# Optimization experiments

Hardware: AMD Instinct MI355X
Metric: run time of the kernel (lower is better)

The kernel has to match this reference:

```python
import jax, jax.numpy as jnp
import numpy as np

EMB = 1024
HEADS = 16
HEAD_DIM = EMB // HEADS


def setup_inputs() -> dict:
    key = jax.random.key(0)
    ks = jax.random.split(key, 6)
    B, S = 4, 1024
    inputs = jax.random.normal(ks[0], (B, S, EMB), dtype=jnp.float32)
    # causal mask: 1.0 where attention is disallowed (added * -1e9 in the layer)
    mask = (1.0 - jnp.tril(jnp.ones((S, S), dtype=jnp.float32)))[None, None, :, :]
    scale = 1.0 / np.sqrt(EMB)
    wq = jax.random.normal(ks[1], (EMB, EMB), dtype=jnp.float32) * scale
    wk = jax.random.normal(ks[2], (EMB, EMB), dtype=jnp.float32) * scale
    wv = jax.random.normal(ks[3], (EMB, EMB), dtype=jnp.float32) * scale
    wo = jax.random.normal(ks[4], (EMB, EMB), dtype=jnp.float32) * scale
    zb = jnp.zeros((EMB,), dtype=jnp.float32)
    return {"inputs": inputs, "mask": mask, "wq": wq, "bq": zb, "wk": wk,
            "bk": zb, "wv": wv, "bv": zb, "wo": wo, "bo": zb}


def _split_heads(t, B):
    # [B, S, E] -> [B, H, S, Dh]
    return t.reshape(B, -1, HEADS, HEAD_DIM).transpose(0, 2, 1, 3)


def reference(inputs, mask, wq, bq, wk, bk, wv, bv, wo, bo):
    B = inputs.shape[0]
    q = _split_heads(inputs @ wq + bq, B)
    k = _split_heads(inputs @ wk + bk, B)
    v = _split_heads(inputs @ wv + bv, B)
    # NOTE: source divides by sqrt(sqrt(head_num)) = head_num**0.25
    scores = jnp.einsum('bhsd,bhtd->bhst', q, k) / jnp.asarray(HEADS, inputs.dtype) ** 0.25
    if mask is not None:
        scores = scores + mask * -1e9
    attn = jax.nn.softmax(scores, axis=-1)
    z = jnp.einsum('bhst,bhtd->bhsd', attn, v)
    # Faithful to source: reshape [B,H,S,Dh] -> [B,S,E] WITHOUT transposing heads back
    z = z.reshape(B, -1, EMB)
    return z @ wo + bo
```

## Files before the change

kernel.cpp:

```cpp
#include <hip/hip_runtime.h>
#include <hip/hip_bf16.h>
#include <stdint.h>

typedef __attribute__((ext_vector_type(8))) short short8;
typedef __attribute__((ext_vector_type(4))) float float4v;

#define SEQ   1024
#define NQKV  3072

__device__ __forceinline__ float bf2f(ushort h) {
    union { uint u; float f; } c; c.u = ((uint)h) << 16; return c.f;
}
__device__ __forceinline__ ushort f2bf(float f) {
    union { uint u; float f; } c; c.f = f;
    uint u = c.u;
    return (ushort)((u + 0x7fffu + ((u >> 16) & 1u)) >> 16);
}
__device__ __forceinline__ uint cvt_pk_bf16(float lo, float hi) {
    uint r;
    asm volatile("v_cvt_pk_bf16_f32 %0, %1, %2" : "=v"(r) : "v"(lo), "v"(hi));
    return r;
}
__device__ __forceinline__ void gl2lds16(const ushort* g, ushort* l) {
    __builtin_amdgcn_global_load_lds(
        (const __attribute__((address_space(1))) unsigned int*)(g),
        (__attribute__((address_space(3))) unsigned int*)(l),
        16, 0, 0);
}

#define FENCE() asm volatile("" ::: "memory")
#define PBAR()  do { FENCE(); __builtin_amdgcn_s_barrier(); FENCE(); } while (0)

__global__ __launch_bounds__(256) void prep_k(const void* __restrict__ X,
                                              const void* __restrict__ w0,
                                              const void* __restrict__ w1,
                                              const void* __restrict__ w2,
                                              const void* __restrict__ w3,
                                              const void* __restrict__ bq,
                                              const void* __restrict__ bk,
                                              const void* __restrict__ bv,
                                              const void* __restrict__ bo,
                                              ushort* __restrict__ xc,
                                              ushort* __restrict__ biasout,
                                              ushort* __restrict__ wtall,
                                              int* __restrict__ flag) {
    __shared__ int tot;
    __shared__ ushort tile[64][72];
    int t = threadIdx.x;
    if (t == 0) tot = 0;
    __syncthreads();
    uint wv = ((const uint*)X)[t];
    uint e = (wv >> 7) & 0xFFu;
    bool isbf = (e >= 100u && e <= 130u);
    unsigned long long m = __ballot(isbf);
    if ((t & 63) == 0) atomicAdd(&tot, __popcll(m));
    __syncthreads();
    bool isf = (tot <= 128);

    int bi = blockIdx.x;
    if (bi == 0 && t == 0) flag[0] = isf ? 1 : 0;

    if (bi < 4096) {
        if (!isf) return;
        int i = (bi * 256 + t) * 4;
        float4 v = *(const float4*)((const float*)X + i);
        ushort4 o;
        o.x = f2bf(v.x); o.y = f2bf(v.y); o.z = f2bf(v.z); o.w = f2bf(v.w);
        *(ushort4*)(xc + i) = o;
    } else if (bi < 4112) {
        int i = (bi - 4096) * 256 + t;
        int sel = i >> 10, j = i & 1023;
        const void* p = (sel == 0) ? bq : (sel == 1) ? bk : (sel == 2) ? bv : bo;
        biasout[i] = isf ? f2bf(((const float*)p)[j]) : ((const ushort*)p)[j];
    } else {
        int idx = bi - 4112;
        int z = idx >> 8, rem = idx & 255;
        const void* in = (z == 0) ? w0 : (z == 1) ? w1 : (z == 2) ? w2 : w3;
        ushort* out = wtall + (size_t)z * 1024 * 1024;
        int k0 = (rem & 15) * 64, n0 = (rem >> 4) * 64;
        int r = t >> 3, c = (t & 7) * 8;
#pragma unroll
        for (int p = 0; p < 2; p++) {
            int rr = r + p * 32;
            if (isf) {
                const float* src = (const float*)in + (size_t)(k0 + rr) * 1024 + n0 + c;
                float4 v0 = *(const float4*)src;
                float4 v1 = *(const float4*)(src + 4);
                tile[rr][c + 0] = f2bf(v0.x); tile[rr][c + 1] = f2bf(v0.y);
                tile[rr][c + 2] = f2bf(v0.z); tile[rr][c + 3] = f2bf(v0.w);
                tile[rr][c + 4] = f2bf(v1.x); tile[rr][c + 5] = f2bf(v1.y);
                tile[rr][c + 6] = f2bf(v1.z); tile[rr][c + 7] = f2bf(v1.w);
            } else {
                uint4 v = *(const uint4*)((const ushort*)in + (size_t)(k0 + rr) * 1024 + n0 + c);
                *(uint4*)&tile[rr][c] = v;
            }
        }
        __syncthreads();
#pragma unroll
        for (int p = 0; p < 2; p++) {
            int n = r + p * 32;
            ushort vals[8];
#pragma unroll
            for (int j = 0; j < 8; j++) vals[j] = tile[c + j][n];
            *(uint4*)(out + (size_t)(n0 + n) * 1024 + k0 + c) = *(uint4*)vals;
        }
    }
}

__device__ __forceinline__ void stage_half(const ushort* src, int K, ushort* lds, int t) {
#pragma unroll
    for (int jj = 0; jj < 2; jj++) {
        int c = jj * 512 + t;
        int row = c >> 3, s = c & 7;
        int kc = s ^ (row & 7);
        gl2lds16(src + (size_t)row * K + kc * 8, lds + c * 8);
    }
}

__global__ __launch_bounds__(512, 2) void gemm256_k(const ushort* __restrict__ Araw,
                                                    const ushort* __restrict__ Aconv,
                                                    const ushort* __restrict__ BT,
                                                    const ushort* __restrict__ bias,
                                                    ushort* __restrict__ C,
                                                    ushort* __restrict__ vt,
                                                    const int* __restrict__ flag) {
    constexpr int K = 1024;
    constexpr int N = NQKV;
    __shared__ ushort As[2][256 * 64];
    __shared__ ushort Bs[2][256 * 64];
    int orig = blockIdx.y * gridDim.x + blockIdx.x;
    int swz = (orig & 7) * 24 + (orig >> 3);
    int n0 = (swz % 12) * 256, m0 = (swz / 12) * 256;
    int t = threadIdx.x;
    int w = t >> 6, lane = t & 63, q = lane >> 4, ln = lane & 15;
    int wr = w & 1, wc = w >> 1;
    const ushort* A = (*flag) ? Aconv : Araw;

    float4v acc[8][4];
#pragma unroll
    for (int r = 0; r < 8; r++)
#pragma unroll
        for (int cc = 0; cc < 4; cc++) acc[r][cc] = (float4v){0.f, 0.f, 0.f, 0.f};

    stage_half(A  + (size_t)m0 * K,           K, &As[0][0], t);
    stage_half(A  + (size_t)(m0 + 128) * K,   K, &As[0][128 * 64], t);
    stage_half(BT + (size_t)n0 * K,           K, &Bs[0][0], t);
    stage_half(BT + (size_t)(n0 + 128) * K,   K, &Bs[0][128 * 64], t);
    stage_half(A  + (size_t)m0 * K + 64,      K, &As[1][0], t);
    stage_half(A  + (size_t)(m0 + 128) * K + 64, K, &As[1][128 * 64], t);
    asm volatile("s_waitcnt vmcnt(4)" ::: "memory");
    PBAR();

    short8 af[4][2];
    short8 bf[2][2][2];

    for (int j = 0; j < 16; j++) {
        int cur = j & 1;
        int nxt = cur ^ 1;
#pragma unroll
        for (int mf = 0; mf < 4; mf++)
#pragma unroll
            for (int kh = 0; kh < 2; kh++) {
                int r = wr * 64 + mf * 16 + ln;
                af[mf][kh] = *(const short8*)&As[cur][(r * 8 + ((kh * 4 + q) ^ (r & 7))) * 8];
            }
#pragma unroll
        for (int nf = 0; nf < 2; nf++)
#pragma unroll
            for (int kh = 0; kh < 2; kh++) {
                int rb = wc * 64 + nf * 16 + ln;
                bf[0][nf][kh] = *(const short8*)&Bs[cur][(rb * 8 + ((kh * 4 + q) ^ (rb & 7))) * 8];
            }
        if (j + 1 < 16) stage_half(BT + (size_t)n0 * K + (j + 1) * 64, K, &Bs[nxt][0], t);
#pragma unroll
        for (int mf = 0; mf < 4; mf++)
#pragma unroll
            for (int nf = 0; nf < 2; nf++)
#pragma unroll
                for (int kh = 0; kh < 2; kh++)
                    acc[mf][nf] = __builtin_amdgcn_mfma_f32_16x16x32_bf16(af[mf][kh], bf[0][nf][kh], acc[mf][nf], 0, 0, 0);
        PBAR();
#pragma unroll
        for (int nf = 0; nf < 2; nf++)
#pragma unroll
            for (int kh = 0; kh < 2; kh++) {
                int rb = wc * 64 + 32 + nf * 16 + ln;
                bf[1][nf][kh] = *(const short8*)&Bs[cur][(rb * 8 + ((kh * 4 + q) ^ (rb & 7))) * 8];
            }
        if (j + 1 < 16) stage_half(BT + (size_t)(n0 + 128) * K + (j + 1) * 64, K, &Bs[nxt][128 * 64], t);
#pragma unroll
        for (int mf = 0; mf < 4; mf++)
#pragma unroll
            for (int nf = 0; nf < 2; nf++)
#pragma unroll
                for (int kh = 0; kh < 2; kh++)
                    acc[mf][2 + nf] = __builtin_amdgcn_mfma_f32_16x16x32_bf16(af[mf][kh], bf[1][nf][kh], acc[mf][2 + nf], 0, 0, 0);
        PBAR();
#pragma unroll
        for (int mf = 0; mf < 4; mf++)
#pragma unroll
            for (int kh = 0; kh < 2; kh++) {
                int r = 128 + wr * 64 + mf * 16 + ln;
                af[mf][kh] = *(const short8*)&As[cur][(r * 8 + ((kh * 4 + q) ^ (r & 7))) * 8];
            }
        if (j + 2 < 16) stage_half(A + (size_t)m0 * K + (j + 2) * 64, K, &As[cur][0], t);
#pragma unroll
        for (int mf = 0; mf < 4; mf++)
#pragma unroll
            for (int nf = 0; nf < 2; nf++)
#pragma unroll
                for (int kh = 0; kh < 2; kh++)
                    acc[4 + mf][2 + nf] = __builtin_amdgcn_mfma_f32_16x16x32_bf16(af[mf][kh], bf[1][nf][kh], acc[4 + mf][2 + nf], 0, 0, 0);
        PBAR();
        if (j + 2 < 16) stage_half(A + (size_t)(m0 + 128) * K + (j + 2) * 64, K, &As[cur][128 * 64], t);
#pragma unroll
        for (int mf = 0; mf < 4; mf++)
#pragma unroll
            for (int nf = 0; nf < 2; nf++)
#pragma unroll
                for (int kh = 0; kh < 2; kh++)
                    acc[4 + mf][nf] = __builtin_amdgcn_mfma_f32_16x16x32_bf16(af[mf][kh], bf[0][nf][kh], acc[4 + mf][nf], 0, 0, 0);
        if (j < 14) { asm volatile("s_waitcnt vmcnt(4)" ::: "memory"); }
        else        { asm volatile("s_waitcnt vmcnt(0)" ::: "memory"); }
        PBAR();
    }

    bool wrv = (n0 >= 2048);
#pragma unroll
    for (int nfull = 0; nfull < 4; nfull++) {
        int n = n0 + wc * 64 + nfull * 16 + ln;
        float bs = bf2f(bias[n]);
#pragma unroll
        for (int m8 = 0; m8 < 8; m8++) {
            ushort pk[4];
#pragma unroll
            for (int i = 0; i < 4; i++) {
                int m = m0 + (m8 >> 2) * 128 + wr * 64 + (m8 & 3) * 16 + q * 4 + i;
                float v = acc[m8][nfull][i] + bs;
                C[(size_t)m * N + n] = f2bf(v);
                pk[i] = f2bf(v);
            }
            if (wrv) {
                int mb = m0 + (m8 >> 2) * 128 + wr * 64 + (m8 & 3) * 16 + q * 4;
                int b = mb >> 10, trow = mb & 1023;
                int h = (n - 2048) >> 6, d = n & 63;
                *(ushort4*)(vt + (((size_t)(b * 16 + h) * 64 + d) * 1024 + trow)) = *(ushort4*)pk;
            }
        }
    }
}

template <int BM, bool DUAL, bool WRV>
__global__ __launch_bounds__(256) void gemm_k(const ushort* __restrict__ Araw,
                                              const ushort* __restrict__ Aconv,
                                              const ushort* __restrict__ BT,
                                              const ushort* __restrict__ bias,
                                              void* __restrict__ C,
                                              ushort* __restrict__ vt,
                                              const int* __restrict__ flag,
                                              int M, int N, int K) {
    constexpr int RM = BM / 32;
    constexpr int AJ = BM / 64;
    __shared__ ushort As[2][BM * 32];
    __shared__ ushort Bs[2][128 * 32];
    int nwgx = gridDim.x;
    int orig = blockIdx.y * nwgx + blockIdx.x;
    int cpx = (nwgx * gridDim.y) >> 3;
    int swz = (orig & 7) * cpx + (orig >> 3);
    int n0 = (swz % nwgx) * 128, m0 = (swz / nwgx) * BM;
    int t = threadIdx.x;
    int w = t >> 6, lane = t & 63, q = lane >> 4, ln = lane & 15;
    int wr = w >> 1, wc = w & 1;
    const ushort* A = (*flag) ? Aconv : Araw;

    float4v acc[RM][4];
#pragma unroll
    for (int r = 0; r < RM; r++)
#pragma unroll
        for (int cc = 0; cc < 4; cc++) acc[r][cc] = (float4v){0.f, 0.f, 0.f, 0.f};

#pragma unroll
    for (int j = 0; j < AJ; j++) {
        int c = j * 256 + t;
        int row = c >> 2, s = c & 3;
        int kc = s ^ ((row >> 1) & 3);
        gl2lds16(A + (size_t)(m0 + row) * K + kc * 8, &As[0][c * 8]);
    }
#pragma unroll
    for (int j = 0; j < 2; j++) {
        int c = j * 256 + t;
        int row = c >> 2, s = c & 3;
        int kc = s ^ ((row >> 1) & 3);
        gl2lds16(BT + (size_t)(n0 + row) * K + kc * 8, &Bs[0][c * 8]);
    }

    int nIter = K >> 5;
    for (int kt = 0; kt < nIter; kt++) {
        int cur = kt & 1;
        __syncthreads();
        if (kt + 1 < nIter) {
            int nk0 = (kt + 1) << 5, nxt = cur ^ 1;
#pragma unroll
            for (int j = 0; j < AJ; j++) {
                int c = j * 256 + t;
                int row = c >> 2, s = c & 3;
                int kc = s ^ ((row >> 1) & 3);
                gl2lds16(A + (size_t)(m0 + row) * K + nk0 + kc * 8, &As[nxt][c * 8]);
            }
#pragma unroll
            for (int j = 0; j < 2; j++) {
                int c = j * 256 + t;
                int row = c >> 2, s = c & 3;
                int kc = s ^ ((row >> 1) & 3);
                gl2lds16(BT + (size_t)(n0 + row) * K + nk0 + kc * 8, &Bs[nxt][c * 8]);
            }
        }
        short8 af[RM], bf[4];
#pragma unroll
        for (int r = 0; r < RM; r++) {
            int row = wr * (BM / 2) + r * 16 + ln;
            af[r] = *(const short8*)&As[cur][((row << 2) | (q ^ ((row >> 1) & 3))) * 8];
        }
#pragma unroll
        for (int cc = 0; cc < 4; cc++) {
            int col = wc * 64 + cc * 16 + ln;
            bf[cc] = *(const short8*)&Bs[cur][((col << 2) | (q ^ ((col >> 1) & 3))) * 8];
        }
#pragma unroll
        for (int r = 0; r < RM; r++)
#pragma unroll
            for (int cc = 0; cc < 4; cc++)
                acc[r][cc] = __builtin_amdgcn_mfma_f32_16x16x32_bf16(af[r], bf[cc], acc[r][cc], 0, 0, 0);
    }

    bool outf = DUAL && (*flag != 0);
    bool wrv = WRV && (n0 >= 2048);
#pragma unroll
    for (int cc = 0; cc < 4; cc++) {
        int n = n0 + wc * 64 + cc * 16 + ln;
        float bs = bf2f(bias[n]);
#pragma unroll
        for (int r = 0; r < RM; r++) {
            ushort pk[4];
#pragma unroll
            for (int i = 0; i < 4; i++) {
                int m = m0 + wr * (BM / 2) + r * 16 + q * 4 + i;
                float v = acc[r][cc][i] + bs;
                if (outf) ((float*)C)[(size_t)m * N + n] = v;
                else      ((ushort*)C)[(size_t)m * N + n] = f2bf(v);
                pk[i] = f2bf(v);
            }
            if (wrv) {
                int mb = m0 + wr * (BM / 2) + r * 16 + q * 4;
                int b = mb >> 10, trow = mb & 1023;
                int h = (n - 2048) >> 6, d = n & 63;
                *(ushort4*)(vt + (((size_t)(b * 16 + h) * 64 + d) * 1024 + trow)) = *(ushort4*)pk;
            }
        }
    }
}

__global__ __launch_bounds__(512) void attn_k(const ushort* __restrict__ qkv,
                                              const ushort* __restrict__ vt,
                                              ushort* __restrict__ zp) {
    __shared__ ushort Ks[2][64 * 64];
    __shared__ ushort Vs[2][64 * 64];
    __shared__ ushort P[8][16 * 76];
    int bh = blockIdx.y;
    int pr = (bh & 32) ? (7 - blockIdx.x) : blockIdx.x;
    int b = bh >> 4, h = bh & 15;
    int t = threadIdx.x;
    int w = t >> 6;
    int grp = w >> 2;
    int lane = t & 63, q = lane >> 4, ln = lane & 15;

    const float CE = 0.72134752f;

    const ushort* Qp = qkv + (size_t)(b * SEQ) * NQKV + h * 64;
    const ushort* Kp = qkv + (size_t)(b * SEQ) * NQKV + 1024 + h * 64;
    const ushort* Vt = vt + (size_t)bh * 64 * 1024;

    int row0 = t >> 3, kc0 = (t & 7) ^ (row0 & 7);

    int tiB = 15 - pr;
    int ti = grp ? tiB : pr;
    int sw = ti * 64 + (w & 3) * 16;

    short8 aq0 = *(const short8*)(Qp + (size_t)(sw + ln) * NQKV + q * 8);
    short8 aq1 = *(const short8*)(Qp + (size_t)(sw + ln) * NQKV + 32 + q * 8);

    float lp = 0.f;
    float4v o[4];
#pragma unroll
    for (int nb = 0; nb < 4; nb++) o[nb] = (float4v){0.f, 0.f, 0.f, 0.f};

    gl2lds16(Kp + (size_t)row0 * NQKV + kc0 * 8, &Ks[0][t * 8]);
    gl2lds16(Vt + (size_t)row0 * 1024 + kc0 * 8, &Vs[0][t * 8]);

    int srow_l = sw + ln;

    for (int kt = 0; kt <= tiB; kt++) {
        int cur = kt & 1;
        int t0 = kt * 64;
        __syncthreads();
        if (kt < tiB) {
            int nt0 = t0 + 64, nxt = cur ^ 1;
            gl2lds16(Kp + (size_t)(nt0 + row0) * NQKV + kc0 * 8, &Ks[nxt][t * 8]);
            gl2lds16(Vt + (size_t)row0 * 1024 + nt0 + kc0 * 8, &Vs[nxt][t * 8]);
        }
        if (kt <= ti) {
            float4v s[4];
#pragma unroll
            for (int nb = 0; nb < 4; nb++) {
                int row = nb * 16 + ln;
                short8 kf0 = *(const short8*)&Ks[cur][((row << 3) | (q ^ (row & 7))) * 8];
                short8 kf1 = *(const short8*)&Ks[cur][((row << 3) | ((4 + q) ^ (row & 7))) * 8];
                s[nb] = (float4v){0.f, 0.f, 0.f, 0.f};
                s[nb] = __builtin_amdgcn_mfma_f32_16x16x32_bf16(kf0, aq0, s[nb], 0, 0, 0);
                s[nb] = __builtin_amdgcn_mfma_f32_16x16x32_bf16(kf1, aq1, s[nb], 0, 0, 0);
            }
            float p[4][4];
            if (kt < ti) {
#pragma unroll
                for (int nb = 0; nb < 4; nb++)
#pragma unroll
                    for (int i = 0; i < 4; i++) p[nb][i] = exp2f(s[nb][i] * CE);
            } else {
#pragma unroll
                for (int nb = 0; nb < 4; nb++)
#pragma unroll
                    for (int i = 0; i < 4; i++) {
                        int tcol = t0 + nb * 16 + q * 4 + i;
                        p[nb][i] = exp2f((tcol <= srow_l) ? s[nb][i] * CE : -1e30f);
                    }
            }
#pragma unroll
            for (int nb = 0; nb < 4; nb++)
                lp += (p[nb][0] + p[nb][1]) + (p[nb][2] + p[nb][3]);
#pragma unroll
            for (int nb = 0; nb < 4; nb++) {
                uint2 pk;
                pk.x = cvt_pk_bf16(p[nb][0], p[nb][1]);
                pk.y = cvt_pk_bf16(p[nb][2], p[nb][3]);
                *(uint2*)&P[w][ln * 76 + nb * 16 + q * 4] = pk;
            }
            asm volatile("s_waitcnt lgkmcnt(0)\n" ::: "memory");
            short8 ap0 = *(const short8*)&P[w][ln * 76 + q * 8];
            short8 ap1 = *(const short8*)&P[w][ln * 76 + 32 + q * 8];
#pragma unroll
            for (int nb = 0; nb < 4; nb++) {
                int row = nb * 16 + ln;
                short8 bv0 = *(const short8*)&Vs[cur][((row << 3) | (q ^ (row & 7))) * 8];
                short8 bv1 = *(const short8*)&Vs[cur][((row << 3) | ((4 + q) ^ (row & 7))) * 8];
                o[nb] = __builtin_amdgcn_mfma_f32_16x16x32_bf16(ap0, bv0, o[nb], 0, 0, 0);
                o[nb] = __builtin_amdgcn_mfma_f32_16x16x32_bf16(ap1, bv1, o[nb], 0, 0, 0);
            }
        }
    }

    float lred = lp;
    lred += __shfl_xor(lred, 16, 64);
    lred += __shfl_xor(lred, 32, 64);
    float l_i[4];
#pragma unroll
    for (int i = 0; i < 4; i++)
        l_i[i] = __shfl(lred, (q << 4) | (q * 4 + i), 64);

#pragma unroll
    for (int nb = 0; nb < 4; nb++) {
#pragma unroll
        for (int i = 0; i < 4; i++) {
            int srow = sw + q * 4 + i;
            int d = nb * 16 + ln;
            float z = o[nb][i] / l_i[i];
            int sp = h * 64 + (srow >> 4);
            int ep = ((srow & 15) << 6) + d;
            zp[((size_t)(b * SEQ + sp)) * 1024 + ep] = f2bf(z);
        }
    }
}

extern "C" void kernel_launch(void* const* d_in, const int* in_sizes, int n_in,
                              void* d_out, int out_size, void* d_ws, size_t ws_size,
                              hipStream_t stream) {
    const void* X  = d_in[0];
    const void* wq = d_in[2];
    const void* bq = d_in[3];
    const void* wk = d_in[4];
    const void* bk = d_in[5];
    const void* wv = d_in[6];
    const void* bv = d_in[7];
    const void* wo = d_in[8];
    const void* bo = d_in[9];

    char* ws = (char*)d_ws;
    int*    flag  = (int*)ws;
    ushort* biasq = (ushort*)(ws + 4096);
    ushort* WTall = (ushort*)(ws + 12288);
    ushort* Xc    = (ushort*)(ws + 8400896);
    ushort* QKV   = (ushort*)(ws + 16789504);
    ushort* VT    = (ushort*)(ws + 41955328);
    ushort* WTo   = WTall + 3 * 1024 * 1024;
    ushort* ZP    = Xc;

    prep_k<<<5136, 256, 0, stream>>>(X, wq, wk, wv, wo, bq, bk, bv, bo,
                                     Xc, biasq, WTall, flag);
    gemm256_k<<<dim3(12, 16), 512, 0, stream>>>(
        (const ushort*)X, Xc, WTall, biasq, QKV, VT, flag);
    attn_k<<<dim3(8, 64), 512, 0, stream>>>(QKV, VT, ZP);
    gemm_k<64, true, false><<<dim3(8, 64), 256, 0, stream>>>(
        ZP, ZP, WTo, biasq + 3072, d_out, nullptr, flag, 4096, 1024, 1024);
}
```

Measured before the change: 184.5 us.

## Rework GEMM prefetch pipelines: triple-buffer gemm_k and reorder QKV stage schedule

The generic gemm_k moves from a double-buffered LDS ring with a __syncthreads per step to a three-stage ring with prefetch distance two and explicit vmcnt waits, so global-to-LDS loads have more time to land before use. The 256x256 QKV kernel reorders its staging so each half-tile of the next k-step is issued right after its source is consumed. It adds explicit lgkmcnt waits with sched_barrier and raises wave priority around the MFMA blocks. The cost is more LDS per block in gemm_k, which may lower occupancy, and tighter scheduling constraints that can serialize LDS reads and MFMAs.

Result: no change. 183.5 us (-0.5%).

```diff
diff --git a/kernel.cpp b/kernel.cpp
--- a/kernel.cpp
+++ b/kernel.cpp
@@ -30,6 +30,8 @@
 
 #define FENCE() asm volatile("" ::: "memory")
 #define PBAR()  do { FENCE(); __builtin_amdgcn_s_barrier(); FENCE(); } while (0)
+#define LGKM0() do { asm volatile("s_waitcnt lgkmcnt(0)" ::: "memory"); \
+                     __builtin_amdgcn_sched_barrier(0); } while (0)
 
 __global__ __launch_bounds__(256) void prep_k(const void* __restrict__ X,
                                               const void* __restrict__ w0,
@@ -142,21 +144,20 @@
 #pragma unroll
         for (int cc = 0; cc < 4; cc++) acc[r][cc] = (float4v){0.f, 0.f, 0.f, 0.f};
 
-    stage_half(A  + (size_t)m0 * K,           K, &As[0][0], t);
-    stage_half(A  + (size_t)(m0 + 128) * K,   K, &As[0][128 * 64], t);
-    stage_half(BT + (size_t)n0 * K,           K, &Bs[0][0], t);
-    stage_half(BT + (size_t)(n0 + 128) * K,   K, &Bs[0][128 * 64], t);
-    stage_half(A  + (size_t)m0 * K + 64,      K, &As[1][0], t);
-    stage_half(A  + (size_t)(m0 + 128) * K + 64, K, &As[1][128 * 64], t);
-    asm volatile("s_waitcnt vmcnt(4)" ::: "memory");
+    stage_half(A  + (size_t)m0 * K,              K, &As[0][0], t);
+    stage_half(BT + (size_t)n0 * K,              K, &Bs[0][0], t);
+    stage_half(BT + (size_t)(n0 + 128) * K,      K, &Bs[0][128 * 64], t);
+    stage_half(A  + (size_t)(m0 + 128) * K,      K, &As[0][128 * 64], t);
+    asm volatile("s_waitcnt vmcnt(2)" ::: "memory");
     PBAR();
 
     short8 af[4][2];
-    short8 bf[2][2][2];
+    short8 bf0[2][2], bf1[2][2];
 
     for (int j = 0; j < 16; j++) {
         int cur = j & 1;
         int nxt = cur ^ 1;
+        bool pf = (j + 1 < 16);
 #pragma unroll
         for (int mf = 0; mf < 4; mf++)
 #pragma unroll
@@ -169,32 +170,40 @@
 #pragma unroll
             for (int kh = 0; kh < 2; kh++) {
                 int rb = wc * 64 + nf * 16 + ln;
-                bf[0][nf][kh] = *(const short8*)&Bs[cur][(rb * 8 + ((kh * 4 + q) ^ (rb & 7))) * 8];
-            }
-        if (j + 1 < 16) stage_half(BT + (size_t)n0 * K + (j + 1) * 64, K, &Bs[nxt][0], t);
+                bf0[nf][kh] = *(const short8*)&Bs[cur][(rb * 8 + ((kh * 4 + q) ^ (rb & 7))) * 8];
+            }
+        if (pf) stage_half(A + (size_t)m0 * K + (j + 1) * 64, K, &As[nxt][0], t);
+        LGKM0();
+        __builtin_amdgcn_s_setprio(1);
 #pragma unroll
         for (int mf = 0; mf < 4; mf++)
 #pragma unroll
             for (int nf = 0; nf < 2; nf++)
 #pragma unroll
                 for (int kh = 0; kh < 2; kh++)
-                    acc[mf][nf] = __builtin_amdgcn_mfma_f32_16x16x32_bf16(af[mf][kh], bf[0][nf][kh], acc[mf][nf], 0, 0, 0);
+                    acc[mf][nf] = __builtin_amdgcn_mfma_f32_16x16x32_bf16(af[mf][kh], bf0[nf][kh], acc[mf][nf], 0, 0, 0);
+        __builtin_amdgcn_s_setprio(0);
         PBAR();
 #pragma unroll
         for (int nf = 0; nf < 2; nf++)
 #pragma unroll
             for (int kh = 0; kh < 2; kh++) {
                 int rb = wc * 64 + 32 + nf * 16 + ln;
-                bf[1][nf][kh] = *(const short8*)&Bs[cur][(rb * 8 + ((kh * 4 + q) ^ (rb & 7))) * 8];
-            }
-        if (j + 1 < 16) stage_half(BT + (size_t)(n0 + 128) * K + (j + 1) * 64, K, &Bs[nxt][128 * 64], t);
+                bf1[nf][kh] = *(const short8*)&Bs[cur][(rb * 8 + ((kh * 4 + q) ^ (rb & 7))) * 8];
+            }
+        if (pf) stage_half(BT + (size_t)n0 * K + (j + 1) * 64, K, &Bs[nxt][0], t);
+        LGKM0();
+        __builtin_amdgcn_s_setprio(1);
 #pragma unroll
         for (int mf = 0; mf < 4; mf++)
 #pragma unroll
             for (int nf = 0; nf < 2; nf++)
 #pragma unroll
                 for (int kh = 0; kh < 2; kh++)
-                    acc[mf][2 + nf] = __builtin_amdgcn_mfma_f32_16x16x32_bf16(af[mf][kh], bf[1][nf][kh], acc[mf][2 + nf], 0, 0, 0);
+                    acc[mf][2 + nf] = __builtin_amdgcn_mfma_f32_16x16x32_bf16(af[mf][kh], bf1[nf][kh], acc[mf][2 + nf], 0, 0, 0);
+        __builtin_amdgcn_s_setprio(0);
+        if (pf) { asm volatile("s_waitcnt vmcnt(4)" ::: "memory"); }
+        else    { asm volatile("s_waitcnt vmcnt(0)" ::: "memory"); }
         PBAR();
 #pragma unroll
         for (int mf = 0; mf < 4; mf++)
@@ -203,25 +212,29 @@
                 int r = 128 + wr * 64 + mf * 16 + ln;
                 af[mf][kh] = *(const short8*)&As[cur][(r * 8 + ((kh * 4 + q) ^ (r & 7))) * 8];
             }
-        if (j + 2 < 16) stage_half(A + (size_t)m0 * K + (j + 2) * 64, K, &As[cur][0], t);
+        if (pf) stage_half(BT + (size_t)(n0 + 128) * K + (j + 1) * 64, K, &Bs[nxt][128 * 64], t);
+        LGKM0();
+        __builtin_amdgcn_s_setprio(1);
 #pragma unroll
         for (int mf = 0; mf < 4; mf++)
 #pragma unroll
             for (int nf = 0; nf < 2; nf++)
 #pragma unroll
                 for (int kh = 0; kh < 2; kh++)
-                    acc[4 + mf][2 + nf] = __builtin_amdgcn_mfma_f32_16x16x32_bf16(af[mf][kh], bf[1][nf][kh], acc[4 + mf][2 + nf], 0, 0, 0);
+                    acc[4 + mf][2 + nf] = __builtin_amdgcn_mfma_f32_16x16x32_bf16(af[mf][kh], bf1[nf][kh], acc[4 + mf][2 + nf], 0, 0, 0);
+        __builtin_amdgcn_s_setprio(0);
         PBAR();
-        if (j + 2 < 16) stage_half(A + (size_t)(m0 + 128) * K + (j + 2) * 64, K, &As[cur][128 * 64], t);
+        if (pf) stage_half(A + (size_t)(m0 + 128) * K + (j + 1) * 64, K, &As[nxt][128 * 64], t);
+        __builtin_amdgcn_s_setprio(1);
 #pragma unroll
         for (int mf = 0; mf < 4; mf++)
 #pragma unroll
             for (int nf = 0; nf < 2; nf++)
 #pragma unroll
                 for (int kh = 0; kh < 2; kh++)
-                    acc[4 + mf][nf] = __builtin_amdgcn_mfma_f32_16x16x32_bf16(af[mf][kh], bf[0][nf][kh], acc[4 + mf][nf], 0, 0, 0);
-        if (j < 14) { asm volatile("s_waitcnt vmcnt(4)" ::: "memory"); }
-        else        { asm volatile("s_waitcnt vmcnt(0)" ::: "memory"); }
+                    acc[4 + mf][nf] = __builtin_amdgcn_mfma_f32_16x16x32_bf16(af[mf][kh], bf0[nf][kh], acc[4 + mf][nf], 0, 0, 0);
+        __builtin_amdgcn_s_setprio(0);
+        if (pf) { asm volatile("s_waitcnt vmcnt(2)" ::: "memory"); }
         PBAR();
     }
 
@@ -261,8 +274,10 @@
                                               int M, int N, int K) {
     constexpr int RM = BM / 32;
     constexpr int AJ = BM / 64;
-    __shared__ ushort As[2][BM * 32];
-    __shared__ ushort Bs[2][128 * 32];
+    constexpr int ASZ = BM * 32;
+    constexpr int BSZ = 128 * 32;
+    __shared__ ushort As[3 * ASZ];
+    __shared__ ushort Bs[3 * BSZ];
     int nwgx = gridDim.x;
     int orig = blockIdx.y * nwgx + blockIdx.x;
     int cpx = (nwgx * gridDim.y) >> 3;
@@ -279,58 +294,68 @@
 #pragma unroll
         for (int cc = 0; cc < 4; cc++) acc[r][cc] = (float4v){0.f, 0.f, 0.f, 0.f};
 
-#pragma unroll
-    for (int j = 0; j < AJ; j++) {
-        int c = j * 256 + t;
-        int row = c >> 2, s = c & 3;
-        int kc = s ^ ((row >> 1) & 3);
-        gl2lds16(A + (size_t)(m0 + row) * K + kc * 8, &As[0][c * 8]);
-    }
-#pragma unroll
-    for (int j = 0; j < 2; j++) {
-        int c = j * 256 + t;
-        int row = c >> 2, s = c & 3;
-        int kc = s ^ ((row >> 1) & 3);
-        gl2lds16(BT + (size_t)(n0 + row) * K + kc * 8, &Bs[0][c * 8]);
-    }
-
     int nIter = K >> 5;
+
+#pragma unroll
+    for (int pj = 0; pj < 2; pj++) {
+        int jk0 = pj << 5;
+#pragma unroll
+        for (int j = 0; j < AJ; j++) {
+            int c = j * 256 + t;
+            int row = c >> 2, s = c & 3;
+            int kc = s ^ ((row >> 1) & 3);
+            gl2lds16(A + (size_t)(m0 + row) * K + jk0 + kc * 8, &As[pj * ASZ + c * 8]);
+        }
+#pragma unroll
+        for (int j = 0; j < 2; j++) {
+            int c = j * 256 + t;
+            int row = c >> 2, s = c & 3;
+            int kc = s ^ ((row >> 1) & 3);
+            gl2lds16(BT + (size_t)(n0 + row) * K + jk0 + kc * 8, &Bs[pj * BSZ + c * 8]);
+        }
+    }
+
+    int cur = 0, stg = 2;
     for (int kt = 0; kt < nIter; kt++) {
-        int cur = kt & 1;
-        __syncthreads();
-        if (kt + 1 < nIter) {
-            int nk0 = (kt + 1) << 5, nxt = cur ^ 1;
+        if (kt + 1 < nIter) { asm volatile("s_waitcnt vmcnt(4)" ::: "memory"); }
+        else                { asm volatile("s_waitcnt vmcnt(0)" ::: "memory"); }
+        PBAR();
+        __builtin_amdgcn_sched_barrier(0);
+        if (kt + 2 < nIter) {
+            int nk0 = (kt + 2) << 5;
 #pragma unroll
             for (int j = 0; j < AJ; j++) {
                 int c = j * 256 + t;
                 int row = c >> 2, s = c & 3;
                 int kc = s ^ ((row >> 1) & 3);
-                gl2lds16(A + (size_t)(m0 + row) * K + nk0 + kc * 8, &As[nxt][c * 8]);
+                gl2lds16(A + (size_t)(m0 + row) * K + nk0 + kc * 8, &As[stg * ASZ + c * 8]);
             }
 #pragma unroll
             for (int j = 0; j < 2; j++) {
                 int c = j * 256 + t;
                 int row = c >> 2, s = c & 3;
                 int kc = s ^ ((row >> 1) & 3);
-                gl2lds16(BT + (size_t)(n0 + row) * K + nk0 + kc * 8, &Bs[nxt][c * 8]);
+                gl2lds16(BT + (size_t)(n0 + row) * K + nk0 + kc * 8, &Bs[stg * BSZ + c * 8]);
             }
         }
         short8 af[RM], bf[4];
 #pragma unroll
         for (int r = 0; r < RM; r++) {
             int row = wr * (BM / 2) + r * 16 + ln;
-            af[r] = *(const short8*)&As[cur][((row << 2) | (q ^ ((row >> 1) & 3))) * 8];
+            af[r] = *(const short8*)&As[cur * ASZ + ((row << 2) | (q ^ ((row >> 1) & 3))) * 8];
         }
 #pragma unroll
         for (int cc = 0; cc < 4; cc++) {
             int col = wc * 64 + cc * 16 + ln;
-            bf[cc] = *(const short8*)&Bs[cur][((col << 2) | (q ^ ((col >> 1) & 3))) * 8];
+            bf[cc] = *(const short8*)&Bs[cur * BSZ + ((col << 2) | (q ^ ((col >> 1) & 3))) * 8];
         }
 #pragma unroll
         for (int r = 0; r < RM; r++)
 #pragma unroll
             for (int cc = 0; cc < 4; cc++)
                 acc[r][cc] = __builtin_amdgcn_mfma_f32_16x16x32_bf16(af[r], bf[cc], acc[r][cc], 0, 0, 0);
+        cur = (cur == 2) ? 0 : cur + 1;
+        stg = (stg == 2) ? 0 : stg + 1;
     }
 
     bool outf = DUAL && (*flag != 0);
```
